# Optimization experiments

Hardware: AMD Instinct MI355X
Metric: run time of the kernel (lower is better)

## Reference

```python
import jax, jax.numpy as jnp
import numpy as np

B = 4096
N_PATCH = 196  # (28/2)^2


def _rx(theta):
    # theta [...] -> RX matrix [..., 2, 2] complex64
    c = jnp.cos(theta / 2) + 0j
    s = -1j * jnp.sin(theta / 2)
    return jnp.stack([jnp.stack([c, s], -1), jnp.stack([s, c], -1)], -2).astype(jnp.complex64)


def _rot(phi, theta, omega):
    # PennyLane Rot(phi, theta, omega) = RZ(omega) RY(theta) RZ(phi), returns [2,2] complex64
    ct = jnp.cos(theta / 2)
    st = jnp.sin(theta / 2)
    m00 = jnp.exp(-1j * (phi + omega) / 2) * ct
    m01 = -jnp.exp(1j * (phi - omega) / 2) * st
    m10 = jnp.exp(-1j * (phi - omega) / 2) * st
    m11 = jnp.exp(1j * (phi + omega) / 2) * ct
    return jnp.stack([jnp.stack([m00, m01]), jnp.stack([m10, m11])]).astype(jnp.complex64)


def _apply_shared(state, U, w):
    # state [N,2,2,2,2], U [2,2] shared across batch, acting on wire w
    s = jnp.moveaxis(state, 1 + w, -1)
    s = jnp.einsum('...a,ba->...b', s, U)
    return jnp.moveaxis(s, -1, 1 + w)


def _apply_batched(state, U, w):
    # U [N,2,2] per-sample gate
    s = jnp.moveaxis(state, 1 + w, -1)
    s = jnp.einsum('n...a,nba->n...b', s, U)
    return jnp.moveaxis(s, -1, 1 + w)


def _cnot(state, c, t):
    s = jnp.moveaxis(state, (1 + c, 1 + t), (-2, -1))
    s = jnp.stack([s[..., 0, :], s[..., 1, ::-1]], axis=-2)
    return jnp.moveaxis(s, (-2, -1), (1 + c, 1 + t))


def _quanv(patches, wq):
    # patches [N,4] angles; wq [n_app, n_layers, 4, 3]
    N = patches.shape[0]
    state = jnp.zeros((N, 16), jnp.complex64).at[:, 0].set(1.0).reshape(N, 2, 2, 2, 2)
    for w in range(4):  # AngleEmbedding: RX per wire
        state = _apply_batched(state, _rx(patches[:, w]), w)
    ranges = (1, 2)  # SEL default: (l % (n_wires-1)) + 1
    for app in range(wq.shape[0]):
        for l in range(wq.shape[1]):
            for w in range(4):
                state = _apply_shared(state, _rot(wq[app, l, w, 0], wq[app, l, w, 1], wq[app, l, w, 2]), w)
            r = ranges[l]
            for w in range(4):
                state = _cnot(state, w, (w + r) % 4)
    p = jnp.abs(state) ** 2  # [N,2,2,2,2]
    feats = []
    for w in range(4):  # <Z_w> = P(bit_w=0) - P(bit_w=1)
        axes = tuple(a for a in range(1, 5) if a != 1 + w)
        m = p.sum(axes)
        feats.append(m[:, 0] - m[:, 1])
    return jnp.stack(feats, -1)  # [N,4]


def _qfc(params, wfc):
    # 1-qubit circuit: RX embedding then Rot gates only (SEL has no entanglers on 1 wire)
    Bq = params.shape[0]
    state = jnp.zeros((Bq, 2), jnp.complex64).at[:, 0].set(1.0)
    state = jnp.einsum('na,nba->nb', state, _rx(params[:, 0]))
    for app in range(wfc.shape[0]):
        for l in range(wfc.shape[1]):
            U = _rot(wfc[app, l, 0, 0], wfc[app, l, 0, 1], wfc[app, l, 0, 2])
            state = jnp.einsum('na,ba->nb', state, U)
    p = jnp.abs(state) ** 2
    return p[:, 0] - p[:, 1]  # [B]


def setup_inputs() -> dict:
    key = jax.random.key(0)
    k1, k2, k3, k4 = jax.random.split(key, 4)
    return {
        'x': jax.random.normal(k1, (B, 784), jnp.float32),
        'weights_q': jax.random.normal(k2, (2, 2, 4, 3), jnp.float32),
        'weights_fc': jax.random.normal(k3, (3, 3, 1, 3), jnp.float32),
        'W_out': jax.random.normal(k4, (10, 1), jnp.float32) * 0.1,
        'b_out': jnp.zeros((10,), jnp.float32),
    }


def reference(x, weights_q, weights_fc, W_out, b_out):
    Bb = x.shape[0]
    img = x.reshape(Bb, 28, 28)
    # extract 2x2 stride-2 patches in (row-block, col-block) order, row-major within patch
    patches = img.reshape(Bb, 14, 2, 14, 2).transpose(0, 1, 3, 2, 4).reshape(Bb * N_PATCH, 4)
    feats = _quanv(patches, weights_q).reshape(Bb, N_PATCH * 4)  # [B,784]
    q = _qfc(feats[:, :1], weights_fc)  # [B]
    logits = q[:, None] @ W_out.T + b_out  # Linear(1,10) -> [B,10]
    return jax.nn.log_softmax(logits, axis=-1)
```

## Files before the change

kernel.cpp:

```cpp
#include <hip/hip_runtime.h>
#include <math.h>


struct c32 { float re, im; };

__device__ __forceinline__ c32 cmul(c32 a, c32 b) {
    return { fmaf(a.re, b.re, -a.im * b.im), fmaf(a.re, b.im, a.im * b.re) };
}
__device__ __forceinline__ c32 cmulc(c32 a, c32 b) {
    return { fmaf(a.re, b.re, a.im * b.im), fmaf(a.re, b.im, -a.im * b.re) };
}
__device__ __forceinline__ c32 cadd(c32 a, c32 b) { return { a.re + b.re, a.im + b.im }; }
__device__ __forceinline__ c32 csub(c32 a, c32 b) { return { a.re - b.re, a.im - b.im }; }

template<int W>
__device__ __forceinline__ void apply1(c32 amp[16], c32 u00, c32 u01, c32 u10, c32 u11) {
    constexpr int s = 8 >> W;
    #pragma unroll
    for (int i = 0; i < 16; ++i) {
        if (i & s) continue;
        c32 a = amp[i], b = amp[i + s];
        amp[i]     = cadd(cmul(u00, a), cmul(u01, b));
        amp[i + s] = cadd(cmul(u10, a), cmul(u11, b));
    }
}

template<int C, int T>
__device__ __forceinline__ void cnot4(c32 amp[16]) {
    constexpr int sc = 8 >> C, st = 8 >> T;
    #pragma unroll
    for (int i = 0; i < 16; ++i) {
        if ((i & sc) && !(i & st)) {
            c32 tmp = amp[i]; amp[i] = amp[i | st]; amp[i | st] = tmp;
        }
    }
}

__device__ __forceinline__ void make_rot(float phi, float th, float om,
                                         c32& u00, c32& u01, c32& u10, c32& u11) {
    float sh, ch; sincosf(th * 0.5f, &sh, &ch);
    float spo, cpo; sincosf((phi + om) * 0.5f, &spo, &cpo);
    float spm, cpm; sincosf((phi - om) * 0.5f, &spm, &cpm);
    u00 = {  cpo * ch, -spo * ch };
    u01 = { -cpm * sh, -spm * sh };
    u10 = {  cpm * sh, -spm * sh };
    u11 = {  cpo * ch,  spo * ch };
}

__global__ __launch_bounds__(64)
void quanv_hybrid_kernel(const float* __restrict__ x,
                         const float* __restrict__ wq,
                         const float* __restrict__ wfc,
                         const float* __restrict__ Wout,
                         const float* __restrict__ bout,
                         float* __restrict__ out,
                         int B)
{
    const int tid = threadIdx.x;
    const int b = blockIdx.x * 64 + tid;

    __shared__ c32  gmat[25][4];
    __shared__ float Ur[16][16], Ui[16][16];
    __shared__ float Gq[16][16];
    __shared__ float yz[2];

    if (tid < 25) {
        const float* p = (tid < 16) ? (wq + 3 * tid) : (wfc + 3 * (tid - 16));
        c32 a, bb, c, d;
        make_rot(p[0], p[1], p[2], a, bb, c, d);
        gmat[tid][0] = a; gmat[tid][1] = bb; gmat[tid][2] = c; gmat[tid][3] = d;
    }
    __syncthreads();

    if (tid < 16) {
        c32 amp[16];
        #pragma unroll
        for (int i = 0; i < 16; ++i) amp[i] = { 0.f, 0.f };
        amp[tid].re = 1.f;

        #pragma unroll
        for (int al = 0; al < 4; ++al) {
            apply1<0>(amp, gmat[al*4+0][0], gmat[al*4+0][1], gmat[al*4+0][2], gmat[al*4+0][3]);
            apply1<1>(amp, gmat[al*4+1][0], gmat[al*4+1][1], gmat[al*4+1][2], gmat[al*4+1][3]);
            apply1<2>(amp, gmat[al*4+2][0], gmat[al*4+2][1], gmat[al*4+2][2], gmat[al*4+2][3]);
            apply1<3>(amp, gmat[al*4+3][0], gmat[al*4+3][1], gmat[al*4+3][2], gmat[al*4+3][3]);
            if ((al & 1) == 0) {
                cnot4<0,1>(amp); cnot4<1,2>(amp); cnot4<2,3>(amp); cnot4<3,0>(amp);
            } else {
                cnot4<0,2>(amp); cnot4<1,3>(amp); cnot4<2,0>(amp); cnot4<3,1>(amp);
            }
        }
        #pragma unroll
        for (int i = 0; i < 16; ++i) { Ur[i][tid] = amp[i].re; Ui[i][tid] = amp[i].im; }
    } else if (tid == 16) {
        c32 v00 = {1.f, 0.f}, v01 = {0.f, 0.f}, v10 = {0.f, 0.f}, v11 = {1.f, 0.f};
        #pragma unroll
        for (int g = 0; g < 9; ++g) {
            c32 u00 = gmat[16+g][0], u01 = gmat[16+g][1], u10 = gmat[16+g][2], u11 = gmat[16+g][3];
            c32 n00 = cadd(cmul(u00, v00), cmul(u01, v10));
            c32 n01 = cadd(cmul(u00, v01), cmul(u01, v11));
            c32 n10 = cadd(cmul(u10, v00), cmul(u11, v10));
            c32 n11 = cadd(cmul(u10, v01), cmul(u11, v11));
            v00 = n00; v01 = n01; v10 = n10; v11 = n11;
        }
        float zH = fmaf(v00.re, v00.re, v00.im * v00.im)
                 - fmaf(v10.re, v10.re, v10.im * v10.im);
        c32 h01 = csub(cmulc(v00, v01), cmulc(v10, v11));
        yz[0] = -h01.im; yz[1] = zH;
    }
    __syncthreads();

    #pragma unroll
    for (int e = 0; e < 4; ++e) {
        int n = tid * 4 + e, j = n >> 4, k = n & 15;
        float mre = 0.f, mim = 0.f;
        #pragma unroll
        for (int i = 0; i < 16; ++i) {
            float ar = Ur[i][j], ai = Ui[i][j], br = Ur[i][k], bi = Ui[i][k];
            float re = fmaf(ar, br,  ai * bi);
            float im = fmaf(ar, bi, -ai * br);
            if (i < 8) { mre += re; mim += im; } else { mre -= re; mim -= im; }
        }
        int m = (__popc(j) - __popc(k)) & 3;
        float g = (m == 0) ? mre : (m == 1) ? -mim : (m == 2) ? -mre : mim;
        Gq[j][k] = g;
    }
    __syncthreads();

    if (b >= B) return;

    const float* xb = x + (size_t)b * 784;
    float ang0 = xb[0], ang1 = xb[1], ang2 = xb[28], ang3 = xb[29];

    float s0, c0, s1, c1, s2, c2, s3, c3;
    sincosf(ang0 * 0.5f, &s0, &c0);
    sincosf(ang1 * 0.5f, &s1, &c1);
    sincosf(ang2 * 0.5f, &s2, &c2);
    sincosf(ang3 * 0.5f, &s3, &c3);

    float A[4] = { c0 * c1, c0 * s1, s0 * c1, s0 * s1 };
    float Bv[4] = { c2 * c3, c2 * s3, s2 * c3, s2 * s3 };
    float r[16];
    #pragma unroll
    for (int k = 0; k < 16; ++k) r[k] = A[k >> 2] * Bv[k & 3];

    float z0 = 0.f;
    #pragma unroll
    for (int j = 0; j < 16; ++j) {
        float t = 0.f;
        #pragma unroll
        for (int k = 0; k < 16; ++k) t = fmaf(Gq[j][k], r[k], t);
        z0 = fmaf(r[j], t, z0);
    }

    float sz, cz; sincosf(z0, &sz, &cz);
    float q = fmaf(cz, yz[1], -sz * yz[0]);

    float lg[10], m = -1e30f;
    #pragma unroll
    for (int j = 0; j < 10; ++j) {
        lg[j] = fmaf(q, Wout[j], bout[j]);
        m = fmaxf(m, lg[j]);
    }
    float sum = 0.f;
    #pragma unroll
    for (int j = 0; j < 10; ++j) sum += expf(lg[j] - m);
    float lse = m + logf(sum);

    float* ob = out + (size_t)b * 10;
    #pragma unroll
    for (int j = 0; j < 10; ++j) ob[j] = lg[j] - lse;
}

extern "C" void kernel_launch(void* const* d_in, const int* in_sizes, int n_in,
                              void* d_out, int out_size, void* d_ws, size_t ws_size,
                              hipStream_t stream) {
    const float* x    = (const float*)d_in[0];
    const float* wq   = (const float*)d_in[1];
    const float* wfc  = (const float*)d_in[2];
    const float* Wout = (const float*)d_in[3];
    const float* bout = (const float*)d_in[4];
    float* out = (float*)d_out;

    int B = in_sizes[0] / 784;
    const int threads = 64;
    int blocks = (B + threads - 1) / threads;
    quanv_hybrid_kernel<<<blocks, threads, 0, stream>>>(x, wq, wfc, Wout, bout, out, B);
}
```

Before: 76.16 us.

## Spread each image across 16 lanes with shuffle reductions and hoisted input loads

Each image is now handled by 16 threads instead of one. Each lane computes one row of the quadratic form, and the row sums, the softmax max and the softmax sum are combined with xor shuffles. Blocks grow to 256 threads and cover 16 images each, so there are four times as many blocks, and each block still recomputes the shared unitary setup. The x angles and output weights are loaded before the setup barrier to hide their latency, and output stores become per-lane coalesced writes. The cost is much more redundant per-block setup work spread over many more blocks.

```diff
diff --git a/kernel.cpp b/kernel.cpp
--- a/kernel.cpp
+++ b/kernel.cpp
@@ -47,7 +47,9 @@
     u11 = {  cpo * ch,  spo * ch };
 }
 
-__global__ __launch_bounds__(64)
+#define GP 20
+
+__global__ __launch_bounds__(256)
 void quanv_hybrid_kernel(const float* __restrict__ x,
                          const float* __restrict__ wq,
                          const float* __restrict__ wfc,
@@ -57,12 +59,20 @@
                          int B)
 {
     const int tid = threadIdx.x;
-    const int b = blockIdx.x * 64 + tid;
-
-    __shared__ c32  gmat[25][4];
+    const int j   = tid & 15;
+    const int img = blockIdx.x * 16 + (tid >> 4);
+    const int imgc = (img < B) ? img : (B - 1);
+
+    __shared__ c32   gmat[25][4];
     __shared__ float Ur[16][16], Ui[16][16];
-    __shared__ float Gq[16][16];
+    __shared__ float Gqs[16 * GP];
     __shared__ float yz[2];
+
+    const float* xb = x + (size_t)imgc * 784;
+    float2 a01 = *reinterpret_cast<const float2*>(xb);
+    float2 a23 = *reinterpret_cast<const float2*>(xb + 28);
+    float Wj = (j < 10) ? Wout[j] : 0.f;
+    float bj = (j < 10) ? bout[j] : 0.f;
 
     if (tid < 25) {
         const float* p = (tid < 16) ? (wq + 3 * tid) : (wfc + 3 * (tid - 16));
@@ -110,66 +120,74 @@
     }
     __syncthreads();
 
-    #pragma unroll
-    for (int e = 0; e < 4; ++e) {
-        int n = tid * 4 + e, j = n >> 4, k = n & 15;
+    {
+        int jj = tid >> 4, kk = tid & 15;
         float mre = 0.f, mim = 0.f;
         #pragma unroll
         for (int i = 0; i < 16; ++i) {
-            float ar = Ur[i][j], ai = Ui[i][j], br = Ur[i][k], bi = Ui[i][k];
+            float ar = Ur[i][jj], ai = Ui[i][jj], br = Ur[i][kk], bi = Ui[i][kk];
             float re = fmaf(ar, br,  ai * bi);
             float im = fmaf(ar, bi, -ai * br);
             if (i < 8) { mre += re; mim += im; } else { mre -= re; mim -= im; }
         }
-        int m = (__popc(j) - __popc(k)) & 3;
-        float g = (m == 0) ? mre : (m == 1) ? -mim : (m == 2) ? -mre : mim;
-        Gq[j][k] = g;
+        int m4 = (__popc(jj) - __popc(kk)) & 3;
+        float g = (m4 == 0) ? mre : (m4 == 1) ? -mim : (m4 == 2) ? -mre : mim;
+        Gqs[jj * GP + kk] = g;
     }
     __syncthreads();
 
-    if (b >= B) return;
-
-    const float* xb = x + (size_t)b * 784;
-    float ang0 = xb[0], ang1 = xb[1], ang2 = xb[28], ang3 = xb[29];
-
     float s0, c0, s1, c1, s2, c2, s3, c3;
-    sincosf(ang0 * 0.5f, &s0, &c0);
-    sincosf(ang1 * 0.5f, &s1, &c1);
-    sincosf(ang2 * 0.5f, &s2, &c2);
-    sincosf(ang3 * 0.5f, &s3, &c3);
-
-    float A[4] = { c0 * c1, c0 * s1, s0 * c1, s0 * s1 };
+    sincosf(a01.x * 0.5f, &s0, &c0);
+    sincosf(a01.y * 0.5f, &s1, &c1);
+    sincosf(a23.x * 0.5f, &s2, &c2);
+    sincosf(a23.y * 0.5f, &s3, &c3);
+
+    float A[4]  = { c0 * c1, c0 * s1, s0 * c1, s0 * s1 };
     float Bv[4] = { c2 * c3, c2 * s3, s2 * c3, s2 * s3 };
     float r[16];
     #pragma unroll
     for (int k = 0; k < 16; ++k) r[k] = A[k >> 2] * Bv[k & 3];
 
-    float z0 = 0.f;
-    #pragma unroll
-    for (int j = 0; j < 16; ++j) {
-        float t = 0.f;
-        #pragma unroll
-        for (int k = 0; k < 16; ++k) t = fmaf(Gq[j][k], r[k], t);
-        z0 = fmaf(r[j], t, z0);
-    }
+    const float* gr = &Gqs[j * GP];
+    float4 g0 = *reinterpret_cast<const float4*>(gr + 0);
+    float4 g1 = *reinterpret_cast<const float4*>(gr + 4);
+    float4 g2 = *reinterpret_cast<const float4*>(gr + 8);
+    float4 g3 = *reinterpret_cast<const float4*>(gr + 12);
+    float t = 0.f;
+    t = fmaf(g0.x, r[0],  t); t = fmaf(g0.y, r[1],  t);
+    t = fmaf(g0.z, r[2],  t); t = fmaf(g0.w, r[3],  t);
+    t = fmaf(g1.x, r[4],  t); t = fmaf(g1.y, r[5],  t);
+    t = fmaf(g1.z, r[6],  t); t = fmaf(g1.w, r[7],  t);
+    t = fmaf(g2.x, r[8],  t); t = fmaf(g2.y, r[9],  t);
+    t = fmaf(g2.z, r[10], t); t = fmaf(g2.w, r[11], t);
+    t = fmaf(g3.x, r[12], t); t = fmaf(g3.y, r[13], t);
+    t = fmaf(g3.z, r[14], t); t = fmaf(g3.w, r[15], t);
+
+    float z0 = r[j] * t;
+    z0 += __shfl_xor(z0, 1);
+    z0 += __shfl_xor(z0, 2);
+    z0 += __shfl_xor(z0, 4);
+    z0 += __shfl_xor(z0, 8);
 
     float sz, cz; sincosf(z0, &sz, &cz);
     float q = fmaf(cz, yz[1], -sz * yz[0]);
 
-    float lg[10], m = -1e30f;
-    #pragma unroll
-    for (int j = 0; j < 10; ++j) {
-        lg[j] = fmaf(q, Wout[j], bout[j]);
-        m = fmaxf(m, lg[j]);
-    }
-    float sum = 0.f;
-    #pragma unroll
-    for (int j = 0; j < 10; ++j) sum += expf(lg[j] - m);
+    float lg = (j < 10) ? fmaf(q, Wj, bj) : -1e30f;
+    float m = lg;
+    m = fmaxf(m, __shfl_xor(m, 1));
+    m = fmaxf(m, __shfl_xor(m, 2));
+    m = fmaxf(m, __shfl_xor(m, 4));
+    m = fmaxf(m, __shfl_xor(m, 8));
+
+    float e = (j < 10) ? expf(lg - m) : 0.f;
+    float sum = e;
+    sum += __shfl_xor(sum, 1);
+    sum += __shfl_xor(sum, 2);
+    sum += __shfl_xor(sum, 4);
+    sum += __shfl_xor(sum, 8);
+
     float lse = m + logf(sum);
-
-    float* ob = out + (size_t)b * 10;
-    #pragma unroll
-    for (int j = 0; j < 10; ++j) ob[j] = lg[j] - lse;
+    if (j < 10 && img < B) out[(size_t)img * 10 + j] = lg - lse;
 }
 
 extern "C" void kernel_launch(void* const* d_in, const int* in_sizes, int n_in,
@@ -183,7 +201,6 @@
     float* out = (float*)d_out;
 
     int B = in_sizes[0] / 784;
-    const int threads = 64;
-    int blocks = (B + threads - 1) / threads;
-    quanv_hybrid_kernel<<<blocks, threads, 0, stream>>>(x, wq, wfc, Wout, bout, out, B);
-}
+    int blocks = (B + 15) / 16;
+    quanv_hybrid_kernel<<<blocks, 256, 0, stream>>>(x, wq, wfc, Wout, bout, out, B);
+}
```

New measurement: 74.88 us. Within noise of the previous version (-1.7%).
